# Optimization experiments

Hardware: AMD Instinct MI355X
Metric: run time of the kernel (lower is better)

Reference implementation:

```python
import jax, jax.numpy as jnp
import numpy as np

B, T, H = 256, 512, 256


def setup_inputs() -> dict:
    key = jax.random.key(0)
    ks = jax.random.split(key, 16)
    s_in, s_h = 1.0 / np.sqrt(1.0), 1.0 / np.sqrt(H)

    def u(k, shape, s):
        return jax.random.uniform(k, shape, jnp.float32, -s, s)

    return {
        "x": jax.random.normal(ks[0], (B, T), jnp.float32),
        # LSTMCell 1: input size 1
        "W_ih1": u(ks[1], (4 * H, 1), s_h), "b_ih1": u(ks[2], (4 * H,), s_h),
        "W_hh1": u(ks[3], (4 * H, H), s_h), "b_hh1": u(ks[4], (4 * H,), s_h),
        # LSTMCell 2: input size H
        "W_ih2": u(ks[5], (4 * H, H), s_h), "b_ih2": u(ks[6], (4 * H,), s_h),
        "W_hh2": u(ks[7], (4 * H, H), s_h), "b_hh2": u(ks[8], (4 * H,), s_h),
        # SelfAttention linears
        "Wa1": u(ks[9], (H, H), s_h), "ba1": u(ks[10], (H,), s_h),
        "Wa2": u(ks[11], (H, H), s_h), "ba2": u(ks[12], (H,), s_h),
        # output linear H -> 1
        "Wo": u(ks[13], (1, H), s_h), "bo": u(ks[14], (1,), s_h),
        "future": 0,
    }


def _lstm_cell(h, c, gates):
    i, f, g, o = jnp.split(gates, 4, axis=-1)
    i, f, o = jax.nn.sigmoid(i), jax.nn.sigmoid(f), jax.nn.sigmoid(o)
    g = jnp.tanh(g)
    c = f * c + i * g
    return o * jnp.tanh(c), c


def reference(x, W_ih1, b_ih1, W_hh1, b_hh1, W_ih2, b_ih2, W_hh2, b_hh2,
              Wa1, ba1, Wa2, ba2, Wo, bo, future):
    n, Tt = x.shape
    Hd = W_hh1.shape[1]

    def step_core(h1, c1, h2, c2, x_t):
        # x_t: [B, 1]
        g1 = x_t @ W_ih1.T + b_ih1 + h1 @ W_hh1.T + b_hh1
        h1, c1 = _lstm_cell(h1, c1, g1)
        g2 = h1 @ W_ih2.T + b_ih2 + h2 @ W_hh2.T + b_hh2
        h2, c2 = _lstm_cell(h2, c2, g2)
        # additive self-attention (dropout p=0 -> identity)
        attn = jax.nn.softmax(jnp.tanh(h2 @ Wa1.T + ba1) @ Wa2.T + ba2, axis=-1)
        out = (attn * h2) @ Wo.T + bo  # [B, 1]
        return h1, c1, h2, c2, out

    def step(carry, x_t):
        h1, c1, h2, c2, _ = carry
        h1, c1, h2, c2, out = step_core(h1, c1, h2, c2, x_t)
        return (h1, c1, h2, c2, out), out

    z = jnp.zeros((n, Hd), x.dtype)
    init = (z, z, z, z, jnp.zeros((n, 1), x.dtype))
    xs = x.T[:, :, None]  # [T, B, 1]
    carry, outs = jax.lax.scan(step, init, xs)

    if future > 0:
        def fstep(carry, _):
            h1, c1, h2, c2, out = carry
            h1, c1, h2, c2, out = step_core(h1, c1, h2, c2, out)
            return (h1, c1, h2, c2, out), out
        _, fouts = jax.lax.scan(fstep, carry, None, length=future)
        outs = jnp.concatenate([outs, fouts], axis=0)

    return outs[:, :, 0].T  # [B, T+future]
```

## Files before the change

kernel.cpp:

```cpp
#include <hip/hip_runtime.h>
#include <hip/hip_bf16.h>

#define HD   256
#define TT   512

typedef unsigned short u16;
typedef unsigned int   u32;
typedef unsigned long long u64;
typedef __attribute__((ext_vector_type(8))) short  short8;
typedef __attribute__((ext_vector_type(4))) float  f32x4;

__device__ __forceinline__ float bf2f(u16 v) { return __uint_as_float(((u32)v) << 16); }
__device__ __forceinline__ u16 f2bf(float f) {
    u32 u = __float_as_uint(f);
    u32 r = u + 0x7fffu + ((u >> 16) & 1u);
    return (u16)(r >> 16);
}
__device__ __forceinline__ float sigf(float x)  { return __builtin_amdgcn_rcpf(1.f + __expf(-x)); }
__device__ __forceinline__ float tanhf_(float x){ float e = __expf(-2.f * x);
                                                  return 2.f * __builtin_amdgcn_rcpf(1.f + e) - 1.f; }

__global__ void cvt_bf_kernel(const float* __restrict__ src, u16* __restrict__ dst, int n) {
    int idx = blockIdx.x * 256 + threadIdx.x;
    if (idx < n) dst[idx] = f2bf(src[idx]);
}

__global__ void bias_kernel(const float* __restrict__ a1, const float* __restrict__ b1,
                            const float* __restrict__ a2, const float* __restrict__ b2,
                            float* __restrict__ o1, float* __restrict__ o2) {
    int i = blockIdx.x * 256 + threadIdx.x;
    o1[i] = a1[i] + b1[i];
    o2[i] = a2[i] + b2[i];
}

__device__ __forceinline__ void load_bfrag(const float* __restrict__ W, int row, int kq, short8* bw) {
#pragma unroll
    for (int kk = 0; kk < 8; ++kk) {
        const float* p = W + row * 256 + kk * 32 + kq * 8;
        short8 s;
#pragma unroll
        for (int j = 0; j < 8; ++j) s[j] = (short)f2bf(p[j]);
        bw[kk] = s;
    }
}

__device__ __forceinline__ u64 aload64(const u64* p) {
    return __hip_atomic_load(p, __ATOMIC_RELAXED, __HIP_MEMORY_SCOPE_AGENT);
}
__device__ __forceinline__ void astore32(u32* p, u32 v) {
    __hip_atomic_store(p, v, __ATOMIC_RELAXED, __HIP_MEMORY_SCOPE_AGENT);
}

__device__ __forceinline__ void flag_wait(const u32* flags, int gb, u32 target) {
    if (threadIdx.x < 8) {
        const u32* slot = flags + (gb * 8 + (int)threadIdx.x) * 32;
        int sp = 0;
        while (__hip_atomic_load(slot, __ATOMIC_RELAXED, __HIP_MEMORY_SCOPE_AGENT) < target) {
            if (++sp > (1 << 24)) break;
        }
    }
    __syncthreads();
}

__device__ __forceinline__ void flag_post(u32* flags, int slotidx, u32 val) {
    __syncthreads();
    if (threadIdx.x == 0)
        __hip_atomic_store(flags + slotidx * 32, val, __ATOMIC_RELAXED, __HIP_MEMORY_SCOPE_AGENT);
}

__global__ __launch_bounds__(512) void lstm_persist(
    const float* __restrict__ x,
    const float* __restrict__ Wih1,
    const float* __restrict__ bias1,
    const float* __restrict__ bias2,
    const float* __restrict__ Whh1,
    const float* __restrict__ Wih2,
    const float* __restrict__ Whh2,
    u32* __restrict__ Hb1, u32* __restrict__ Hb2,
    u16* __restrict__ H2out, u32* flags)
{
    __shared__ __align__(16) u16 sh1hi[16 * 264], sh1lo[16 * 264];
    __shared__ __align__(16) u16 sh2hi[16 * 264], sh2lo[16 * 264];
    __shared__ float xs[TT * 16];
    __shared__ float gbuf1[4 * 16 * 36], gbuf2[4 * 16 * 36];
    __shared__ float wihs[128], b1s[128], b2s[128];

    const int tid = threadIdx.x;
    const int blk = blockIdx.x;
    const int gb = blk >> 3, hg = blk & 7;
    const int l = tid & 63, wv = tid >> 6;
    const int g = wv >> 1, hh = wv & 1;
    const int nloc = l & 15, kq = l >> 4;
    const int wrow = g * 256 + hg * 32 + hh * 16 + nloc;

    short8 bW1[8], bW2[8], bW3[8];
    load_bfrag(Whh1, wrow, kq, bW1);
    load_bfrag(Wih2, wrow, kq, bW2);
    load_bfrag(Whh2, wrow, kq, bW3);

    for (int idx = tid; idx < 16 * TT; idx += 512) {
        int b = idx >> 9, t = idx & 511;
        xs[t * 16 + b] = x[(gb * 16 + b) * TT + t];
    }
    if (tid < 128) {
        int rr = (tid >> 5) * 256 + hg * 32 + (tid & 31);
        wihs[tid] = Wih1[rr]; b1s[tid] = bias1[rr]; b2s[tid] = bias2[rr];
    }

    const int cb = tid >> 5, ci = tid & 31;
    const int bg = gb * 16 + cb, ig = hg * 32 + ci;
#pragma unroll
    for (int pp = 0; pp < 2; ++pp) {
        astore32(&Hb1[((pp * 256 + bg) << 8) + ig], 0u);
        astore32(&Hb2[((pp * 256 + bg) << 8) + ig], 0u);
    }
    float c1 = 0.f, c2 = 0.f;

    flag_post(flags, gb * 8 + hg, 1u);

    const int aoff = nloc * 264 + kq * 8;
    const int sb = tid >> 5, scol = (tid & 31) * 8;
    const int sbase = sb * 264 + scol;

    for (int k = 0; k <= TT; ++k) {
        flag_wait(flags, gb, (u32)(k + 1));

        const int rp = k & 1, wp = rp ^ 1;
        {
            const u32* p1 = Hb1 + ((rp * 256 + gb * 16 + sb) << 8) + scol;
            const u32* p2 = Hb2 + ((rp * 256 + gb * 16 + sb) << 8) + scol;
            u32 w1v[8], w2v[8];
#pragma unroll
            for (int j = 0; j < 4; ++j) {
                u64 t = aload64((const u64*)p1 + j);
                w1v[2 * j] = (u32)t; w1v[2 * j + 1] = (u32)(t >> 32);
            }
#pragma unroll
            for (int j = 0; j < 4; ++j) {
                u64 t = aload64((const u64*)p2 + j);
                w2v[2 * j] = (u32)t; w2v[2 * j + 1] = (u32)(t >> 32);
            }
            u32 h1h[4], h1l[4], h2h[4], h2l[4];
#pragma unroll
            for (int i = 0; i < 4; ++i) {
                u32 a = w1v[2 * i], b = w1v[2 * i + 1];
                h1h[i] = (a & 0xffffu) | (b << 16);
                h1l[i] = (a >> 16) | (b & 0xffff0000u);
                a = w2v[2 * i]; b = w2v[2 * i + 1];
                h2h[i] = (a & 0xffffu) | (b << 16);
                h2l[i] = (a >> 16) | (b & 0xffff0000u);
            }
            *(uint4*)(sh1hi + sbase) = *(uint4*)(h1h);
            *(uint4*)(sh1lo + sbase) = *(uint4*)(h1l);
            *(uint4*)(sh2hi + sbase) = *(uint4*)(h2h);
            *(uint4*)(sh2lo + sbase) = *(uint4*)(h2l);
        }
        __syncthreads();

        f32x4 acc1a = {0,0,0,0}, acc1b = {0,0,0,0};
        f32x4 acc2a = {0,0,0,0}, acc2b = {0,0,0,0};
#pragma unroll
        for (int kk = 0; kk < 8; ++kk) {
            short8 a1h = *(const short8*)(sh1hi + aoff + kk * 32);
            short8 a1l = *(const short8*)(sh1lo + aoff + kk * 32);
            if (k < TT) {
                acc1a = __builtin_amdgcn_mfma_f32_16x16x32_bf16(a1h, bW1[kk], acc1a, 0, 0, 0);
                acc1b = __builtin_amdgcn_mfma_f32_16x16x32_bf16(a1l, bW1[kk], acc1b, 0, 0, 0);
            }
            if (k > 0) {
                acc2a = __builtin_amdgcn_mfma_f32_16x16x32_bf16(a1h, bW2[kk], acc2a, 0, 0, 0);
                acc2b = __builtin_amdgcn_mfma_f32_16x16x32_bf16(a1l, bW2[kk], acc2b, 0, 0, 0);
                short8 a2h = *(const short8*)(sh2hi + aoff + kk * 32);
                short8 a2l = *(const short8*)(sh2lo + aoff + kk * 32);
                acc2a = __builtin_amdgcn_mfma_f32_16x16x32_bf16(a2h, bW3[kk], acc2a, 0, 0, 0);
                acc2b = __builtin_amdgcn_mfma_f32_16x16x32_bf16(a2l, bW3[kk], acc2b, 0, 0, 0);
            }
        }
#pragma unroll
        for (int r = 0; r < 4; ++r) {
            int m = (l >> 4) * 4 + r;
            gbuf1[(g * 16 + m) * 36 + hh * 16 + nloc] = acc1a[r] + acc1b[r];
            gbuf2[(g * 16 + m) * 36 + hh * 16 + nloc] = acc2a[r] + acc2b[r];
        }
        __syncthreads();

        u16 hi2 = 0;
        if (k < TT) {
            float xv = xs[k * 16 + cb];
            float g0 = gbuf1[(0 * 16 + cb) * 36 + ci] + xv * wihs[ci]      + b1s[ci];
            float g1 = gbuf1[(1 * 16 + cb) * 36 + ci] + xv * wihs[32 + ci] + b1s[32 + ci];
            float g2 = gbuf1[(2 * 16 + cb) * 36 + ci] + xv * wihs[64 + ci] + b1s[64 + ci];
            float g3 = gbuf1[(3 * 16 + cb) * 36 + ci] + xv * wihs[96 + ci] + b1s[96 + ci];
            float ii = sigf(g0), ff = sigf(g1), gg = tanhf_(g2), oo = sigf(g3);
            c1 = ff * c1 + ii * gg;
            float h = oo * tanhf_(c1);
            u16 hi = f2bf(h); u32 word = (u32)hi | ((u32)f2bf(h - bf2f(hi)) << 16);
            astore32(&Hb1[((wp * 256 + bg) << 8) + ig], word);
        }
        if (k > 0) {
            float g0 = gbuf2[(0 * 16 + cb) * 36 + ci] + b2s[ci];
            float g1 = gbuf2[(1 * 16 + cb) * 36 + ci] + b2s[32 + ci];
            float g2 = gbuf2[(2 * 16 + cb) * 36 + ci] + b2s[64 + ci];
            float g3 = gbuf2[(3 * 16 + cb) * 36 + ci] + b2s[96 + ci];
            float ii = sigf(g0), ff = sigf(g1), gg = tanhf_(g2), oo = sigf(g3);
            c2 = ff * c2 + ii * gg;
            float h = oo * tanhf_(c2);
            hi2 = f2bf(h); u32 word = (u32)hi2 | ((u32)f2bf(h - bf2f(hi2)) << 16);
            astore32(&Hb2[((wp * 256 + bg) << 8) + ig], word);
        }
        flag_post(flags, gb * 8 + hg, (u32)(k + 2));
        if (k > 0) H2out[(bg * TT + (k - 1)) * 256 + ig] = hi2;
    }
}

__global__ __launch_bounds__(256) void attn_fused(
    const u16*  __restrict__ Wa1b, const u16* __restrict__ Wa2b,
    const float* __restrict__ ba1, const float* __restrict__ ba2,
    const float* __restrict__ Wo,  const float* __restrict__ bo,
    const u16*  __restrict__ H2,   float* __restrict__ out)
{
    __shared__ __align__(16) u16 sA[64 * 264];
    __shared__ __align__(16) u16 sP[64 * 264];
    __shared__ float red[64 * 12];
    __shared__ float sb1[256], sb2[256], swo[256];

    const int tid = threadIdx.x;
    const int w = tid >> 6, l = tid & 63;
    const int c = l & 15, q = l >> 4;
    const int row0 = blockIdx.x * 64;

    {
        const int r = tid >> 2, qq = tid & 3;
        const uint4* src = (const uint4*)(H2 + (row0 + r) * 256 + qq * 64);
#pragma unroll
        for (int j = 0; j < 8; ++j) {
            uint4 v = src[j];
            *(uint4*)(sA + r * 264 + qq * 64 + j * 8) = v;
        }
    }
    if (tid < 256) { sb1[tid] = ba1[tid]; sb2[tid] = ba2[tid]; swo[tid] = Wo[tid]; }
    __syncthreads();

    f32x4 acc[4][4];
#pragma unroll
    for (int mi = 0; mi < 4; ++mi)
#pragma unroll
        for (int ni = 0; ni < 4; ++ni) acc[mi][ni] = (f32x4){0,0,0,0};

#pragma unroll
    for (int ni = 0; ni < 4; ++ni) {
        const int row = w * 64 + ni * 16 + c;
        const u16* wp = Wa1b + row * 256 + q * 8;
        short8 bW[8];
#pragma unroll
        for (int kk = 0; kk < 8; ++kk) bW[kk] = *(const short8*)(wp + kk * 32);
#pragma unroll
        for (int kk = 0; kk < 8; ++kk)
#pragma unroll
            for (int mi = 0; mi < 4; ++mi) {
                short8 a = *(const short8*)(sA + (mi * 16 + c) * 264 + q * 8 + kk * 32);
                acc[mi][ni] = __builtin_amdgcn_mfma_f32_16x16x32_bf16(a, bW[kk], acc[mi][ni], 0, 0, 0);
            }
    }
#pragma unroll
    for (int mi = 0; mi < 4; ++mi)
#pragma unroll
        for (int ni = 0; ni < 4; ++ni) {
            const int n = w * 64 + ni * 16 + c;
            const float bj = sb1[n];
#pragma unroll
            for (int r = 0; r < 4; ++r) {
                int m = mi * 16 + q * 4 + r;
                sP[m * 264 + n] = f2bf(tanhf(acc[mi][ni][r] + bj));
            }
        }
    __syncthreads();

#pragma unroll
    for (int mi = 0; mi < 4; ++mi)
#pragma unroll
        for (int ni = 0; ni < 4; ++ni) acc[mi][ni] = (f32x4){0,0,0,0};
#pragma unroll
    for (int ni = 0; ni < 4; ++ni) {
        const int row = w * 64 + ni * 16 + c;
        const u16* wp = Wa2b + row * 256 + q * 8;
        short8 bW[8];
#pragma unroll
        for (int kk = 0; kk < 8; ++kk) bW[kk] = *(const short8*)(wp + kk * 32);
#pragma unroll
        for (int kk = 0; kk < 8; ++kk)
#pragma unroll
            for (int mi = 0; mi < 4; ++mi) {
                short8 a = *(const short8*)(sP + (mi * 16 + c) * 264 + q * 8 + kk * 32);
                acc[mi][ni] = __builtin_amdgcn_mfma_f32_16x16x32_bf16(a, bW[kk], acc[mi][ni], 0, 0, 0);
            }
    }

    float mx[4][4];
#pragma unroll
    for (int mi = 0; mi < 4; ++mi)
#pragma unroll
        for (int r = 0; r < 4; ++r) mx[mi][r] = -1e30f;
#pragma unroll
    for (int mi = 0; mi < 4; ++mi)
#pragma unroll
        for (int ni = 0; ni < 4; ++ni) {
            const float bj = sb2[w * 64 + ni * 16 + c];
#pragma unroll
            for (int r = 0; r < 4; ++r) {
                float s = acc[mi][ni][r] + bj;
                acc[mi][ni][r] = s;
                mx[mi][r] = fmaxf(mx[mi][r], s);
            }
        }
#pragma unroll
    for (int off = 1; off < 16; off <<= 1)
#pragma unroll
        for (int mi = 0; mi < 4; ++mi)
#pragma unroll
            for (int r = 0; r < 4; ++r) mx[mi][r] = fmaxf(mx[mi][r], __shfl_xor(mx[mi][r], off));
    if (c == 0)
#pragma unroll
        for (int mi = 0; mi < 4; ++mi)
#pragma unroll
            for (int r = 0; r < 4; ++r) red[(mi * 16 + q * 4 + r) * 12 + w] = mx[mi][r];
    __syncthreads();
#pragma unroll
    for (int mi = 0; mi < 4; ++mi)
#pragma unroll
        for (int r = 0; r < 4; ++r) {
            const float* rp = red + (mi * 16 + q * 4 + r) * 12;
            mx[mi][r] = fmaxf(fmaxf(rp[0], rp[1]), fmaxf(rp[2], rp[3]));
        }
    float suml[4][4], sumw[4][4];
#pragma unroll
    for (int mi = 0; mi < 4; ++mi)
#pragma unroll
        for (int r = 0; r < 4; ++r) { suml[mi][r] = 0.f; sumw[mi][r] = 0.f; }
#pragma unroll
    for (int mi = 0; mi < 4; ++mi)
#pragma unroll
        for (int ni = 0; ni < 4; ++ni) {
            const int n = w * 64 + ni * 16 + c;
            const float wov = swo[n];
#pragma unroll
            for (int r = 0; r < 4; ++r) {
                int m = mi * 16 + q * 4 + r;
                float e = __expf(acc[mi][ni][r] - mx[mi][r]);
                suml[mi][r] += e;
                sumw[mi][r] += e * bf2f(sA[m * 264 + n]) * wov;
            }
        }
#pragma unroll
    for (int off = 1; off < 16; off <<= 1)
#pragma unroll
        for (int mi = 0; mi < 4; ++mi)
#pragma unroll
            for (int r = 0; r < 4; ++r) {
                suml[mi][r] += __shfl_xor(suml[mi][r], off);
                sumw[mi][r] += __shfl_xor(sumw[mi][r], off);
            }
    __syncthreads();
    if (c == 0)
#pragma unroll
        for (int mi = 0; mi < 4; ++mi)
#pragma unroll
            for (int r = 0; r < 4; ++r) {
                int m = mi * 16 + q * 4 + r;
                red[m * 12 + 4 + w] = suml[mi][r];
                red[m * 12 + 8 + w] = sumw[mi][r];
            }
    __syncthreads();
    if (tid < 64) {
        const float* rp = red + tid * 12;
        float lsum = rp[4] + rp[5] + rp[6] + rp[7];
        float wsum = rp[8] + rp[9] + rp[10] + rp[11];
        out[row0 + tid] = wsum / lsum + bo[0];
    }
}

extern "C" void kernel_launch(void* const* d_in, const int* in_sizes, int n_in,
                              void* d_out, int out_size, void* d_ws, size_t ws_size,
                              hipStream_t stream) {
    const float* x    = (const float*)d_in[0];
    const float* Wih1 = (const float*)d_in[1];
    const float* bih1 = (const float*)d_in[2];
    const float* Whh1 = (const float*)d_in[3];
    const float* bhh1 = (const float*)d_in[4];
    const float* Wih2 = (const float*)d_in[5];
    const float* bih2 = (const float*)d_in[6];
    const float* Whh2 = (const float*)d_in[7];
    const float* bhh2 = (const float*)d_in[8];
    const float* Wa1  = (const float*)d_in[9];
    const float* ba1  = (const float*)d_in[10];
    const float* Wa2  = (const float*)d_in[11];
    const float* ba2  = (const float*)d_in[12];
    const float* Wo   = (const float*)d_in[13];
    const float* bo   = (const float*)d_in[14];

    char* ws = (char*)d_ws;
    u16*   Wa1b  = (u16*)(ws + 0);
    u16*   Wa2b  = (u16*)(ws + 131072);
    float* bias1 = (float*)(ws + 262144);
    float* bias2 = (float*)(ws + 266240);
    u32*   flags = (u32*)(ws + 270336);
    u32*   Hb1   = (u32*)(ws + 524288);
    u32*   Hb2   = (u32*)(ws + 1048576);
    u16*   H2    = (u16*)(ws + 2097152);
    float* out   = (float*)d_out;

    (void)hipMemsetAsync(flags, 0, 16384, stream);
    bias_kernel<<<4, 256, 0, stream>>>(bih1, bhh1, bih2, bhh2, bias1, bias2);
    cvt_bf_kernel<<<256, 256, 0, stream>>>(Wa1, Wa1b, 65536);
    cvt_bf_kernel<<<256, 256, 0, stream>>>(Wa2, Wa2b, 65536);

    lstm_persist<<<128, 512, 0, stream>>>(x, Wih1, bias1, bias2,
                                          Whh1, Wih2, Whh2, Hb1, Hb2, H2, flags);
    attn_fused<<<2048, 256, 0, stream>>>(Wa1b, Wa2b, ba1, ba2, Wo, bo, H2, out);
}
```

Before: 2.219 ms.

## Widen LSTM persistent blocks to 1024 threads, halving cross-block flag groups

Each persistent LSTM block now owns 64 hidden units instead of 32, using 16 waves and 1024 threads, so each batch group spans 4 blocks instead of 8. Each step then waits on fewer flags, and fewer blocks reload the shared hidden state, which cuts inter-block synchronisation and redundant global traffic per time step. In exchange, only 64 CUs are used, each block does more MFMA and gate work per step, and the larger block raises register pressure: three weight fragment arrays are held per thread under a 1024-thread launch bound.

```diff
diff --git a/kernel.cpp b/kernel.cpp
--- a/kernel.cpp
+++ b/kernel.cpp
@@ -52,8 +52,8 @@
 }
 
 __device__ __forceinline__ void flag_wait(const u32* flags, int gb, u32 target) {
-    if (threadIdx.x < 8) {
-        const u32* slot = flags + (gb * 8 + (int)threadIdx.x) * 32;
+    if (threadIdx.x < 4) {
+        const u32* slot = flags + (gb * 4 + (int)threadIdx.x) * 32;
         int sp = 0;
         while (__hip_atomic_load(slot, __ATOMIC_RELAXED, __HIP_MEMORY_SCOPE_AGENT) < target) {
             if (++sp > (1 << 24)) break;
@@ -68,7 +68,7 @@
         __hip_atomic_store(flags + slotidx * 32, val, __ATOMIC_RELAXED, __HIP_MEMORY_SCOPE_AGENT);
 }
 
-__global__ __launch_bounds__(512) void lstm_persist(
+__global__ __launch_bounds__(1024) void lstm_persist(
     const float* __restrict__ x,
     const float* __restrict__ Wih1,
     const float* __restrict__ bias1,
@@ -82,33 +82,33 @@
     __shared__ __align__(16) u16 sh1hi[16 * 264], sh1lo[16 * 264];
     __shared__ __align__(16) u16 sh2hi[16 * 264], sh2lo[16 * 264];
     __shared__ float xs[TT * 16];
-    __shared__ float gbuf1[4 * 16 * 36], gbuf2[4 * 16 * 36];
-    __shared__ float wihs[128], b1s[128], b2s[128];
+    __shared__ float gbuf1[4 * 16 * 68], gbuf2[4 * 16 * 68];
+    __shared__ float wihs[256], b1s[256], b2s[256];
 
     const int tid = threadIdx.x;
     const int blk = blockIdx.x;
-    const int gb = blk >> 3, hg = blk & 7;
+    const int gb = blk >> 2, hg = blk & 3;
     const int l = tid & 63, wv = tid >> 6;
-    const int g = wv >> 1, hh = wv & 1;
+    const int g = wv >> 2, cg = wv & 3;
     const int nloc = l & 15, kq = l >> 4;
-    const int wrow = g * 256 + hg * 32 + hh * 16 + nloc;
+    const int wrow = g * 256 + hg * 64 + cg * 16 + nloc;
 
     short8 bW1[8], bW2[8], bW3[8];
     load_bfrag(Whh1, wrow, kq, bW1);
     load_bfrag(Wih2, wrow, kq, bW2);
     load_bfrag(Whh2, wrow, kq, bW3);
 
-    for (int idx = tid; idx < 16 * TT; idx += 512) {
+    for (int idx = tid; idx < 16 * TT; idx += 1024) {
         int b = idx >> 9, t = idx & 511;
         xs[t * 16 + b] = x[(gb * 16 + b) * TT + t];
     }
-    if (tid < 128) {
-        int rr = (tid >> 5) * 256 + hg * 32 + (tid & 31);
+    if (tid < 256) {
+        int rr = (tid >> 6) * 256 + hg * 64 + (tid & 63);
         wihs[tid] = Wih1[rr]; b1s[tid] = bias1[rr]; b2s[tid] = bias2[rr];
     }
 
-    const int cb = tid >> 5, ci = tid & 31;
-    const int bg = gb * 16 + cb, ig = hg * 32 + ci;
+    const int cb = tid >> 6, ci = tid & 63;
+    const int bg = gb * 16 + cb, ig = hg * 64 + ci;
 #pragma unroll
     for (int pp = 0; pp < 2; ++pp) {
         astore32(&Hb1[((pp * 256 + bg) << 8) + ig], 0u);
@@ -116,10 +116,10 @@
     }
     float c1 = 0.f, c2 = 0.f;
 
-    flag_post(flags, gb * 8 + hg, 1u);
+    flag_post(flags, gb * 4 + hg, 1u);
 
     const int aoff = nloc * 264 + kq * 8;
-    const int sb = tid >> 5, scol = (tid & 31) * 8;
+    const int sb = tid >> 6, scol = (tid & 63) * 4;
     const int sbase = sb * 264 + scol;
 
     for (int k = 0; k <= TT; ++k) {
@@ -129,31 +129,21 @@
         {
             const u32* p1 = Hb1 + ((rp * 256 + gb * 16 + sb) << 8) + scol;
             const u32* p2 = Hb2 + ((rp * 256 + gb * 16 + sb) << 8) + scol;
-            u32 w1v[8], w2v[8];
-#pragma unroll
-            for (int j = 0; j < 4; ++j) {
-                u64 t = aload64((const u64*)p1 + j);
-                w1v[2 * j] = (u32)t; w1v[2 * j + 1] = (u32)(t >> 32);
-            }
-#pragma unroll
-            for (int j = 0; j < 4; ++j) {
-                u64 t = aload64((const u64*)p2 + j);
-                w2v[2 * j] = (u32)t; w2v[2 * j + 1] = (u32)(t >> 32);
-            }
-            u32 h1h[4], h1l[4], h2h[4], h2l[4];
-#pragma unroll
-            for (int i = 0; i < 4; ++i) {
-                u32 a = w1v[2 * i], b = w1v[2 * i + 1];
-                h1h[i] = (a & 0xffffu) | (b << 16);
-                h1l[i] = (a >> 16) | (b & 0xffff0000u);
-                a = w2v[2 * i]; b = w2v[2 * i + 1];
-                h2h[i] = (a & 0xffffu) | (b << 16);
-                h2l[i] = (a >> 16) | (b & 0xffff0000u);
-            }
-            *(uint4*)(sh1hi + sbase) = *(uint4*)(h1h);
-            *(uint4*)(sh1lo + sbase) = *(uint4*)(h1l);
-            *(uint4*)(sh2hi + sbase) = *(uint4*)(h2h);
-            *(uint4*)(sh2lo + sbase) = *(uint4*)(h2l);
+            u64 t10 = aload64((const u64*)p1);
+            u64 t11 = aload64((const u64*)p1 + 1);
+            u64 t20 = aload64((const u64*)p2);
+            u64 t21 = aload64((const u64*)p2 + 1);
+            u32 w0 = (u32)t10, w1 = (u32)(t10 >> 32), w2 = (u32)t11, w3 = (u32)(t11 >> 32);
+            uint2 vhi, vlo;
+            vhi.x = (w0 & 0xffffu) | (w1 << 16);  vhi.y = (w2 & 0xffffu) | (w3 << 16);
+            vlo.x = (w0 >> 16) | (w1 & 0xffff0000u);  vlo.y = (w2 >> 16) | (w3 & 0xffff0000u);
+            *(uint2*)(sh1hi + sbase) = vhi;
+            *(uint2*)(sh1lo + sbase) = vlo;
+            w0 = (u32)t20; w1 = (u32)(t20 >> 32); w2 = (u32)t21; w3 = (u32)(t21 >> 32);
+            vhi.x = (w0 & 0xffffu) | (w1 << 16);  vhi.y = (w2 & 0xffffu) | (w3 << 16);
+            vlo.x = (w0 >> 16) | (w1 & 0xffff0000u);  vlo.y = (w2 >> 16) | (w3 & 0xffff0000u);
+            *(uint2*)(sh2hi + sbase) = vhi;
+            *(uint2*)(sh2lo + sbase) = vlo;
         }
         __syncthreads();
 
@@ -178,19 +168,19 @@
         }
 #pragma unroll
         for (int r = 0; r < 4; ++r) {
-            int m = (l >> 4) * 4 + r;
-            gbuf1[(g * 16 + m) * 36 + hh * 16 + nloc] = acc1a[r] + acc1b[r];
-            gbuf2[(g * 16 + m) * 36 + hh * 16 + nloc] = acc2a[r] + acc2b[r];
+            int m = kq * 4 + r;
+            gbuf1[(g * 16 + m) * 68 + cg * 16 + nloc] = acc1a[r] + acc1b[r];
+            gbuf2[(g * 16 + m) * 68 + cg * 16 + nloc] = acc2a[r] + acc2b[r];
         }
         __syncthreads();
 
         u16 hi2 = 0;
         if (k < TT) {
             float xv = xs[k * 16 + cb];
-            float g0 = gbuf1[(0 * 16 + cb) * 36 + ci] + xv * wihs[ci]      + b1s[ci];
-            float g1 = gbuf1[(1 * 16 + cb) * 36 + ci] + xv * wihs[32 + ci] + b1s[32 + ci];
-            float g2 = gbuf1[(2 * 16 + cb) * 36 + ci] + xv * wihs[64 + ci] + b1s[64 + ci];
-            float g3 = gbuf1[(3 * 16 + cb) * 36 + ci] + xv * wihs[96 + ci] + b1s[96 + ci];
+            float g0 = gbuf1[(0 * 16 + cb) * 68 + ci] + xv * wihs[ci]       + b1s[ci];
+            float g1 = gbuf1[(1 * 16 + cb) * 68 + ci] + xv * wihs[64 + ci]  + b1s[64 + ci];
+            float g2 = gbuf1[(2 * 16 + cb) * 68 + ci] + xv * wihs[128 + ci] + b1s[128 + ci];
+            float g3 = gbuf1[(3 * 16 + cb) * 68 + ci] + xv * wihs[192 + ci] + b1s[192 + ci];
             float ii = sigf(g0), ff = sigf(g1), gg = tanhf_(g2), oo = sigf(g3);
             c1 = ff * c1 + ii * gg;
             float h = oo * tanhf_(c1);
@@ -198,17 +188,17 @@
             astore32(&Hb1[((wp * 256 + bg) << 8) + ig], word);
         }
         if (k > 0) {
-            float g0 = gbuf2[(0 * 16 + cb) * 36 + ci] + b2s[ci];
-            float g1 = gbuf2[(1 * 16 + cb) * 36 + ci] + b2s[32 + ci];
-            float g2 = gbuf2[(2 * 16 + cb) * 36 + ci] + b2s[64 + ci];
-            float g3 = gbuf2[(3 * 16 + cb) * 36 + ci] + b2s[96 + ci];
+            float g0 = gbuf2[(0 * 16 + cb) * 68 + ci] + b2s[ci];
+            float g1 = gbuf2[(1 * 16 + cb) * 68 + ci] + b2s[64 + ci];
+            float g2 = gbuf2[(2 * 16 + cb) * 68 + ci] + b2s[128 + ci];
+            float g3 = gbuf2[(3 * 16 + cb) * 68 + ci] + b2s[192 + ci];
             float ii = sigf(g0), ff = sigf(g1), gg = tanhf_(g2), oo = sigf(g3);
             c2 = ff * c2 + ii * gg;
             float h = oo * tanhf_(c2);
             hi2 = f2bf(h); u32 word = (u32)hi2 | ((u32)f2bf(h - bf2f(hi2)) << 16);
             astore32(&Hb2[((wp * 256 + bg) << 8) + ig], word);
         }
-        flag_post(flags, gb * 8 + hg, (u32)(k + 2));
+        flag_post(flags, gb * 4 + hg, (u32)(k + 2));
         if (k > 0) H2out[(bg * TT + (k - 1)) * 256 + ig] = hi2;
     }
 }
@@ -414,7 +404,7 @@
     cvt_bf_kernel<<<256, 256, 0, stream>>>(Wa1, Wa1b, 65536);
     cvt_bf_kernel<<<256, 256, 0, stream>>>(Wa2, Wa2b, 65536);
 
-    lstm_persist<<<128, 512, 0, stream>>>(x, Wih1, bias1, bias2,
+    lstm_persist<<<64, 1024, 0, stream>>>(x, Wih1, bias1, bias2,
                                           Whh1, Wih2, Whh2, Hb1, Hb2, H2, flags);
     attn_fused<<<2048, 256, 0, stream>>>(Wa1b, Wa2b, ba1, ba2, Wo, bo, H2, out);
 }
```

New measurement: 3.439 ms. 1.55x slower.
